# Optimization experiments

Hardware: AMD Instinct MI355X
Metric: run time of the kernel (lower is better)

## Reference

```python
import jax, jax.numpy as jnp
import numpy as np

SCALE = 2
KSIZE = 3
EPS = 0.2  # damping constant in 1/(grad^2 + 0.2)


def _unfold_patches(x, k):
    """x: [B, C, H, W] -> [B, C, k*k, H, W], zero-padded, row-major window order
    (matches torch.nn.functional.unfold channel ordering)."""
    B, C, H, W = x.shape
    p = k // 2
    xp = jnp.pad(x, ((0, 0), (0, 0), (p, p), (p, p)))
    return jnp.stack(
        [xp[:, :, i:i + H, j:j + W] for i in range(k) for j in range(k)], axis=2
    )


def setup_inputs() -> dict:
    key = jax.random.key(0)
    x = jax.random.normal(key, (4, 128, 128, 128), dtype=jnp.float32)
    return {"x": x}


def reference(x):
    B, C, H, W = x.shape
    k, s = KSIZE, SCALE
    k2 = k * k

    # channel-mean map [B, 1, H, W]
    mean = jnp.mean(x, axis=1, keepdims=True)

    # local gradients of the mean map: unfold(mean) - mean  -> [B, k2, H, W]
    grad = _unfold_patches(mean, k)[:, 0] - mean
    grad = 1.0 / (grad * grad + EPS)

    # nearest-neighbor upsample by s (F.interpolate default mode='nearest')
    up = jnp.repeat(jnp.repeat(grad, s, axis=2), s, axis=3)  # [B, k2, Hs, Ws]
    kernels = jax.nn.softmax(up, axis=1)

    # CARAFE content-aware reassembly (group=1):
    # output pixel (i, j) gathers the kxk neighborhood of source pixel
    # (i//s, j//s) of x and reduces it with kernels[:, :, i, j].
    patches = _unfold_patches(x, k)                 # [B, C, k2, H, W]
    Kr = kernels.reshape(B, k2, H, s, W, s)         # split upsampled grid
    out = jnp.einsum('bkhpwq,bckhw->bchpwq', Kr, patches)
    return out.reshape(B, C, H * s, W * s)
```

## Files before the change

### kernel.cpp

```cpp
#include <hip/hip_runtime.h>

#define NB 4
#define NC 128
#define NH 128
#define NW 128
#define EPSV 0.2f
#define TH 2

typedef float v4f __attribute__((ext_vector_type(4)));

__global__ __launch_bounds__(512) void fused_carafe(const float* __restrict__ x,
                                                    float* __restrict__ out) {
    const int chunk = gridDim.x >> 3;
    const int bid = blockIdx.x;
    const int swz = (bid & 7) * chunk + (bid >> 3);
    const int b  = swz >> 6;
    const int h0 = (swz & 63) * TH;

    __shared__ float mrow[4][NW];
    __shared__ float wgt[TH][9][NW];

    const int tid = threadIdx.x;

    {
        const int r = tid >> 7;
        const int w = tid & 127;
        const int hh = h0 - 1 + r;
        float s = 0.f;
        if (hh >= 0 && hh < NH) {
            const float* px = x + ((size_t)b * NC * NH + hh) * NW + w;
            #pragma unroll 16
            for (int c = 0; c < NC; ++c)
                s += px[(size_t)c * NH * NW];
        }
        mrow[r][w] = s * (1.0f / NC);
    }
    __syncthreads();

    if (tid < 256) {
        const int r = tid >> 7;
        const int w = tid & 127;
        const float mc = mrow[r + 1][w];
        float v[9];
        float vmax = -1e30f;
        #pragma unroll
        for (int ky = 0; ky < 3; ++ky) {
            #pragma unroll
            for (int kx = -1; kx <= 1; ++kx) {
                const int ww = w + kx;
                const float mp = (ww >= 0 && ww < NW) ? mrow[r + ky][ww] : 0.f;
                const float g = mp - mc;
                const float val = 1.0f / (g * g + EPSV);
                v[ky * 3 + kx + 1] = val;
                vmax = fmaxf(vmax, val);
            }
        }
        float sum = 0.f;
        #pragma unroll
        for (int k = 0; k < 9; ++k) { v[k] = __expf(v[k] - vmax); sum += v[k]; }
        const float rs = 1.0f / sum;
        #pragma unroll
        for (int k = 0; k < 9; ++k) wgt[r][k][w] = v[k] * rs;
    }
    __syncthreads();

    const int wp = tid & 63;
    const int cg = tid >> 6;
    const int wa = 2 * wp;

    float wA0[9], wB0[9], wA1[9], wB1[9];
    #pragma unroll
    for (int k = 0; k < 9; ++k) {
        wA0[k] = wgt[0][k][wa];  wB0[k] = wgt[0][k][wa + 1];
        wA1[k] = wgt[1][k][wa];  wB1[k] = wgt[1][k][wa + 1];
    }

    const bool rv0 = (h0 > 0), rv3 = (h0 + 2 < NH);
    const bool tv0 = (wp > 0), tv3 = (wp < 63);

    #pragma unroll 2
    for (int i = 0; i < 16; ++i) {
        const int c = cg * 16 + i;
        const float* xc = x + ((size_t)(b * NC + c)) * (NH * NW);

        float a[4][4];
        #pragma unroll
        for (int rr = 0; rr < 4; ++rr) {
            const int hh = h0 - 1 + rr;
            const bool rv = (rr == 0) ? rv0 : ((rr == 3) ? rv3 : true);
            const float* row = xc + hh * NW + wa;
            a[rr][0] = (rv && tv0) ? row[-1] : 0.f;
            a[rr][1] = rv ? row[0] : 0.f;
            a[rr][2] = rv ? row[1] : 0.f;
            a[rr][3] = (rv && tv3) ? row[2] : 0.f;
        }

        float v0a = 0.f, v0b = 0.f, v1a = 0.f, v1b = 0.f;
        #pragma unroll
        for (int ky = 0; ky < 3; ++ky) {
            #pragma unroll
            for (int kx = 0; kx < 3; ++kx) {
                const int k = ky * 3 + kx;
                v0a += wA0[k] * a[ky][kx];
                v0b += wB0[k] * a[ky][kx + 1];
                v1a += wA1[k] * a[ky + 1][kx];
                v1b += wB1[k] * a[ky + 1][kx + 1];
            }
        }

        float* o = out + ((size_t)(b * NC + c) * (NH * 2) + 2 * h0) * (NW * 2) + 4 * wp;
        const v4f p0 = {v0a, v0a, v0b, v0b};
        const v4f p1 = {v1a, v1a, v1b, v1b};
        __builtin_nontemporal_store(p0, (v4f*)(o));
        __builtin_nontemporal_store(p0, (v4f*)(o + (NW * 2)));
        __builtin_nontemporal_store(p1, (v4f*)(o + 2 * (NW * 2)));
        __builtin_nontemporal_store(p1, (v4f*)(o + 3 * (NW * 2)));
    }
}

extern "C" void kernel_launch(void* const* d_in, const int* in_sizes, int n_in,
                              void* d_out, int out_size, void* d_ws, size_t ws_size,
                              hipStream_t stream) {
    const float* x = (const float*)d_in[0];
    float* out = (float*)d_out;
    fused_carafe<<<dim3(NB * NH / TH), dim3(512), 0, stream>>>(x, out);
}
```

Measured before the change: 33.95 us.

## Split channel-mean into separate kernel and widen carafe blocks to 1024 threads

Moves the channel-mean computation into its own kernel that writes a mean map to workspace, replacing the fused version that re-read four rows of all channels in every block (about 2x redundant reads of x). The carafe kernel now reads the mean map from global memory and uses 1024 threads, with 8 channels per thread group instead of 16. The cost is an extra kernel launch and a small global round trip for the mean map, plus different occupancy from the larger blocks.

```diff
diff --git a/kernel.cpp b/kernel.cpp
--- a/kernel.cpp
+++ b/kernel.cpp
@@ -9,49 +9,71 @@
 
 typedef float v4f __attribute__((ext_vector_type(4)));
 
-__global__ __launch_bounds__(512) void fused_carafe(const float* __restrict__ x,
-                                                    float* __restrict__ out) {
+__global__ __launch_bounds__(256) void mean_kernel(const float* __restrict__ x,
+                                                   float* __restrict__ mean) {
+    const int tid = threadIdx.x;
+    const int pos = tid & 31;
+    const int cg  = tid >> 5;
+    const int gpos = blockIdx.x * 32 + pos;
+    const int b    = gpos >> 12;
+    const int pos4 = gpos & 4095;
+
+    const float4* x4 = (const float4*)x;
+    float4 acc = make_float4(0.f, 0.f, 0.f, 0.f);
+    const int cbase = (b * NC + cg * 16) * (NH * NW / 4) + pos4;
+    #pragma unroll
+    for (int cc = 0; cc < 16; ++cc) {
+        float4 v = x4[cbase + cc * (NH * NW / 4)];
+        acc.x += v.x; acc.y += v.y; acc.z += v.z; acc.w += v.w;
+    }
+
+    __shared__ float4 red[256];
+    red[tid] = acc;
+    __syncthreads();
+    if (tid < 32) {
+        float4 s = red[tid];
+        #pragma unroll
+        for (int g = 1; g < 8; ++g) {
+            float4 v = red[tid + 32 * g];
+            s.x += v.x; s.y += v.y; s.z += v.z; s.w += v.w;
+        }
+        const float inv = 1.0f / NC;
+        s.x *= inv; s.y *= inv; s.z *= inv; s.w *= inv;
+        ((float4*)mean)[blockIdx.x * 32 + tid] = s;
+    }
+}
+
+__global__ __launch_bounds__(1024) void carafe_kernel(const float* __restrict__ x,
+                                                      const float* __restrict__ mean,
+                                                      float* __restrict__ out) {
     const int chunk = gridDim.x >> 3;
     const int bid = blockIdx.x;
     const int swz = (bid & 7) * chunk + (bid >> 3);
     const int b  = swz >> 6;
     const int h0 = (swz & 63) * TH;
 
-    __shared__ float mrow[4][NW];
     __shared__ float wgt[TH][9][NW];
 
     const int tid = threadIdx.x;
-
-    {
-        const int r = tid >> 7;
-        const int w = tid & 127;
-        const int hh = h0 - 1 + r;
-        float s = 0.f;
-        if (hh >= 0 && hh < NH) {
-            const float* px = x + ((size_t)b * NC * NH + hh) * NW + w;
-            #pragma unroll 16
-            for (int c = 0; c < NC; ++c)
-                s += px[(size_t)c * NH * NW];
-        }
-        mrow[r][w] = s * (1.0f / NC);
-    }
-    __syncthreads();
+    const float* mb = mean + (size_t)b * NH * NW;
 
     if (tid < 256) {
         const int r = tid >> 7;
         const int w = tid & 127;
-        const float mc = mrow[r + 1][w];
+        const int h = h0 + r;
+        const float mc = mb[h * NW + w];
         float v[9];
         float vmax = -1e30f;
         #pragma unroll
-        for (int ky = 0; ky < 3; ++ky) {
+        for (int ky = -1; ky <= 1; ++ky) {
             #pragma unroll
             for (int kx = -1; kx <= 1; ++kx) {
-                const int ww = w + kx;
-                const float mp = (ww >= 0 && ww < NW) ? mrow[r + ky][ww] : 0.f;
+                const int hh = h + ky, ww = w + kx;
+                const float mp = (hh >= 0 && hh < NH && ww >= 0 && ww < NW)
+                                     ? mb[hh * NW + ww] : 0.0f;
                 const float g = mp - mc;
                 const float val = 1.0f / (g * g + EPSV);
-                v[ky * 3 + kx + 1] = val;
+                v[(ky + 1) * 3 + (kx + 1)] = val;
                 vmax = fmaxf(vmax, val);
             }
         }
@@ -79,8 +101,8 @@
     const bool tv0 = (wp > 0), tv3 = (wp < 63);
 
     #pragma unroll 2
-    for (int i = 0; i < 16; ++i) {
-        const int c = cg * 16 + i;
+    for (int i = 0; i < 8; ++i) {
+        const int c = cg * 8 + i;
         const float* xc = x + ((size_t)(b * NC + c)) * (NH * NW);
 
         float a[4][4];
@@ -123,5 +145,8 @@
                               hipStream_t stream) {
     const float* x = (const float*)d_in[0];
     float* out = (float*)d_out;
-    fused_carafe<<<dim3(NB * NH / TH), dim3(512), 0, stream>>>(x, out);
+    float* mean = (float*)d_ws;
+
+    mean_kernel<<<dim3(512), dim3(256), 0, stream>>>(x, mean);
+    carafe_kernel<<<dim3(NB * NH / TH), dim3(1024), 0, stream>>>(x, mean, out);
 }
```

New measurement: 39.17 us. +15.4%, slower.

## Compute channel means once per row via grid sync instead of recomputing halos

Applied to the files above, without the earlier changes.

Each block now computes the channel mean only for its own two rows, splitting the channel sum across both halves of the block, and writes the result to a workspace buffer. A cooperative grid-wide sync follows, after which each block reads its four needed mean rows, including halo rows, from that buffer. This removes the redundant halo mean computation, which had each block reading 4 rows across all channels instead of 2. The cost is a cooperative launch, a grid barrier and a global round trip for the means.

```diff
diff --git a/kernel.cpp b/kernel.cpp
--- a/kernel.cpp
+++ b/kernel.cpp
@@ -1,4 +1,7 @@
 #include <hip/hip_runtime.h>
+#include <hip/hip_cooperative_groups.h>
+
+namespace cg = cooperative_groups;
 
 #define NB 4
 #define NC 128
@@ -10,6 +13,7 @@
 typedef float v4f __attribute__((ext_vector_type(4)));
 
 __global__ __launch_bounds__(512) void fused_carafe(const float* __restrict__ x,
+                                                    float* __restrict__ meanbuf,
                                                     float* __restrict__ out) {
     const int chunk = gridDim.x >> 3;
     const int bid = blockIdx.x;
@@ -17,23 +21,40 @@
     const int b  = swz >> 6;
     const int h0 = (swz & 63) * TH;
 
+    __shared__ float partial[2][2][NW];
     __shared__ float mrow[4][NW];
     __shared__ float wgt[TH][9][NW];
 
     const int tid = threadIdx.x;
 
     {
+        const int w    = tid & 127;
+        const int r    = (tid >> 7) & 1;
+        const int half = tid >> 8;
+        const int h = h0 + r;
+        const float* px = x + (((size_t)(b * NC + half * 64)) * NH + h) * NW + w;
+        float s = 0.f;
+        #pragma unroll 16
+        for (int c = 0; c < 64; ++c)
+            s += px[(size_t)c * NH * NW];
+        partial[half][r][w] = s;
+    }
+    __syncthreads();
+    if (tid < 256) {
+        const int w = tid & 127;
         const int r = tid >> 7;
+        const float m = (partial[0][r][w] + partial[1][r][w]) * (1.0f / NC);
+        meanbuf[((size_t)b * NH + h0 + r) * NW + w] = m;
+    }
+
+    cg::this_grid().sync();
+
+    {
         const int w = tid & 127;
+        const int r = tid >> 7;
         const int hh = h0 - 1 + r;
-        float s = 0.f;
-        if (hh >= 0 && hh < NH) {
-            const float* px = x + ((size_t)b * NC * NH + hh) * NW + w;
-            #pragma unroll 16
-            for (int c = 0; c < NC; ++c)
-                s += px[(size_t)c * NH * NW];
-        }
-        mrow[r][w] = s * (1.0f / NC);
+        mrow[r][w] = (hh >= 0 && hh < NH)
+                         ? meanbuf[((size_t)b * NH + hh) * NW + w] : 0.f;
     }
     __syncthreads();
 
@@ -65,7 +86,7 @@
     __syncthreads();
 
     const int wp = tid & 63;
-    const int cg = tid >> 6;
+    const int cg_ = tid >> 6;
     const int wa = 2 * wp;
 
     float wA0[9], wB0[9], wA1[9], wB1[9];
@@ -80,7 +101,7 @@
 
     #pragma unroll 2
     for (int i = 0; i < 16; ++i) {
-        const int c = cg * 16 + i;
+        const int c = cg_ * 16 + i;
         const float* xc = x + ((size_t)(b * NC + c)) * (NH * NW);
 
         float a[4][4];
@@ -123,5 +144,9 @@
                               hipStream_t stream) {
     const float* x = (const float*)d_in[0];
     float* out = (float*)d_out;
-    fused_carafe<<<dim3(NB * NH / TH), dim3(512), 0, stream>>>(x, out);
+    float* meanbuf = (float*)d_ws;
+
+    void* args[] = {(void*)&x, (void*)&meanbuf, (void*)&out};
+    hipLaunchCooperativeKernel((void*)fused_carafe, dim3(NB * NH / TH), dim3(512),
+                               args, 0, stream);
 }
```

Measured after the change: 64.23 us. 89.2% more time.

## Share channel-mean rows across blocks via global buffer and neighbor flags

Applied to the files above, without the earlier changes.

Before, each block recomputed the channel mean for four rows, which includes the halo rows its neighbors also compute. Now each block computes only its own two rows, split over channel groups and reduced in shared memory. It writes them to a global workspace and waits on release/acquire flags from the adjacent blocks before reading the halo rows. This cuts redundant channel-sum reads of x but adds a spin-wait dependency between blocks, which can deadlock if neighbors are not co-resident, plus an extra memset launch.

```diff
diff --git a/kernel.cpp b/kernel.cpp
--- a/kernel.cpp
+++ b/kernel.cpp
@@ -8,32 +8,70 @@
 #define TH 2
 
 typedef float v4f __attribute__((ext_vector_type(4)));
+typedef float v2f __attribute__((ext_vector_type(2)));
 
 __global__ __launch_bounds__(512) void fused_carafe(const float* __restrict__ x,
+                                                    float* __restrict__ meanbuf,
+                                                    int* __restrict__ flags,
                                                     float* __restrict__ out) {
     const int chunk = gridDim.x >> 3;
     const int bid = blockIdx.x;
     const int swz = (bid & 7) * chunk + (bid >> 3);
     const int b  = swz >> 6;
-    const int h0 = (swz & 63) * TH;
+    const int pr = swz & 63;
+    const int h0 = pr * TH;
 
+    __shared__ v2f part[2][4][64];
     __shared__ float mrow[4][NW];
     __shared__ float wgt[TH][9][NW];
 
     const int tid = threadIdx.x;
 
     {
+        const int w2 = tid & 63;
+        const int cg = (tid >> 6) & 3;
+        const int r  = tid >> 8;
+        const float* px = x + (((size_t)(b * NC + cg * 32)) * NH + (h0 + r)) * NW + 2 * w2;
+        v2f s = {0.f, 0.f};
+        #pragma unroll 8
+        for (int c = 0; c < 32; ++c) {
+            v2f v = *(const v2f*)(px + (size_t)c * NH * NW);
+            s.x += v.x; s.y += v.y;
+        }
+        part[r][cg][w2] = s;
+    }
+    __syncthreads();
+    if (tid < 128) {
+        const int w2 = tid & 63;
+        const int r  = tid >> 6;
+        v2f s = part[r][0][w2];
+        #pragma unroll
+        for (int g = 1; g < 4; ++g) { v2f v = part[r][g][w2]; s.x += v.x; s.y += v.y; }
+        s.x *= (1.0f / NC); s.y *= (1.0f / NC);
+        *(v2f*)(meanbuf + ((size_t)b * NH + h0 + r) * NW + 2 * w2) = s;
+    }
+    __syncthreads();
+    __threadfence();
+    if (tid == 0)
+        __hip_atomic_store(&flags[swz], 1, __ATOMIC_RELEASE, __HIP_MEMORY_SCOPE_AGENT);
+    if (tid < 2) {
+        const int dir = tid ? 1 : -1;
+        const bool need = tid ? (pr < 63) : (pr > 0);
+        if (need) {
+            const int nb = swz + dir;
+            while (__hip_atomic_load(&flags[nb], __ATOMIC_ACQUIRE,
+                                     __HIP_MEMORY_SCOPE_AGENT) == 0)
+                __builtin_amdgcn_s_sleep(1);
+        }
+    }
+    __syncthreads();
+
+    {
+        const int w = tid & 127;
         const int r = tid >> 7;
-        const int w = tid & 127;
         const int hh = h0 - 1 + r;
-        float s = 0.f;
-        if (hh >= 0 && hh < NH) {
-            const float* px = x + ((size_t)b * NC * NH + hh) * NW + w;
-            #pragma unroll 16
-            for (int c = 0; c < NC; ++c)
-                s += px[(size_t)c * NH * NW];
-        }
-        mrow[r][w] = s * (1.0f / NC);
+        mrow[r][w] = (hh >= 0 && hh < NH)
+                         ? meanbuf[((size_t)b * NH + hh) * NW + w] : 0.f;
     }
     __syncthreads();
 
@@ -65,7 +103,7 @@
     __syncthreads();
 
     const int wp = tid & 63;
-    const int cg = tid >> 6;
+    const int cg_ = tid >> 6;
     const int wa = 2 * wp;
 
     float wA0[9], wB0[9], wA1[9], wB1[9];
@@ -80,7 +118,7 @@
 
     #pragma unroll 2
     for (int i = 0; i < 16; ++i) {
-        const int c = cg * 16 + i;
+        const int c = cg_ * 16 + i;
         const float* xc = x + ((size_t)(b * NC + c)) * (NH * NW);
 
         float a[4][4];
@@ -123,5 +161,11 @@
                               hipStream_t stream) {
     const float* x = (const float*)d_in[0];
     float* out = (float*)d_out;
-    fused_carafe<<<dim3(NB * NH / TH), dim3(512), 0, stream>>>(x, out);
+    float* meanbuf = (float*)d_ws;
+    int* flags = (int*)((char*)d_ws + NB * NH * NW * 4);
+
+    hipMemsetAsync(flags, 0, NB * (NH / TH) * sizeof(int), stream);
+    void* kargs_x = (void*)x;
+    fused_carafe<<<dim3(NB * NH / TH), dim3(512), 0, stream>>>(x, meanbuf, flags, out);
+    (void)kargs_x;
 }
```

Measured after the change: 72.58 us. 2.14x slower.
